# Kernel optimization log

Hardware: AMD Instinct MI355X
Metric: run time of the kernel (lower is better)

## Reference

```python
import jax, jax.numpy as jnp
import numpy as np

N = 8192          # total nodes (bipartite: first half left, second half right)
E = 65536         # raw edges
D = 256           # emb_dim
H = 8             # heads
HD = D // H       # head_dim = 32
EAD = 2           # edge_attr_dim


def _init(k, shape, fan_in):
    return (jax.random.normal(k, shape, jnp.float32) / np.sqrt(fan_in)).astype(jnp.float32)


def setup_inputs() -> dict:
    key = jax.random.key(0)
    ks = jax.random.split(key, 16)
    x = jax.random.normal(ks[0], (N, D), jnp.float32)
    src = jax.random.randint(ks[1], (E,), 0, N // 2, jnp.int32)
    dst = jax.random.randint(ks[2], (E,), N // 2, N, jnp.int32)
    edge_index = jnp.stack([src, dst])                       # [2, E]
    edge_attr = jax.random.uniform(ks[3], (E, EAD), jnp.float32)
    query_mask = jax.random.randint(ks[4], (E,), 0, 2, jnp.int32).astype(bool)
    return {
        "x": x,
        "edge_index": edge_index,
        "edge_attr": edge_attr,
        "query_mask": query_mask,
        "start_right": N // 2,
        "W_kqv": _init(ks[5], (D, 3 * D), D), "b_kqv": jnp.zeros((3 * D,), jnp.float32),
        "W_edge": _init(ks[6], (EAD, D), EAD), "b_edge": jnp.zeros((D,), jnp.float32),
        "W_att1": _init(ks[7], (3 * HD, HD), 3 * HD), "b_att1": jnp.zeros((HD,), jnp.float32),
        "W_att2": _init(ks[8], (HD, 1), HD), "b_att2": jnp.zeros((1,), jnp.float32),
        "W_out": _init(ks[9], (D, D), D), "b_out": jnp.zeros((D,), jnp.float32),
        "bn_gamma": jnp.ones((D,), jnp.float32), "bn_beta": jnp.zeros((D,), jnp.float32),
    }


def _build_graph(edge_index, query_mask, n):
    """Replicates MetaGNN.forward edge preprocessing (static, int-only)."""
    ei = np.asarray(edge_index)
    qm = np.asarray(query_mask).astype(bool)
    sup = np.where(~qm)[0]                                   # support edges
    # cat([edge_index[:, support], edge_index.flip(0)], dim=1)
    src = np.concatenate([ei[0, sup], ei[1]])
    dst = np.concatenate([ei[1, sup], ei[0]])
    attr_idx = np.concatenate([sup, np.arange(ei.shape[1])])
    # remove_self_loops
    keep = src != dst
    src, dst, attr_idx = src[keep], dst[keep], attr_idx[keep]
    # add_self_loops with fill_value [0, 0]
    loops = np.arange(n)
    src = np.concatenate([src, loops])
    dst = np.concatenate([dst, loops])
    return jnp.asarray(src), jnp.asarray(dst), jnp.asarray(attr_idx)


def _layer(x, src, dst, ea, W_kqv, b_kqv, W_edge, b_edge, W_att1, b_att1,
           W_att2, b_att2, W_out, b_out, bn_gamma, bn_beta):
    n = x.shape[0]
    kqv = x @ W_kqv + b_kqv                                  # [N, 3D]
    q = kqv[dst, :D].reshape(-1, H, HD)                      # x_i (target)
    k = kqv[src, D:2 * D].reshape(-1, H, HD) / np.sqrt(HD)   # x_j (source)
    v = kqv[src, 2 * D:].reshape(-1, H, HD)
    ef = jax.nn.relu((ea @ W_edge + b_edge).reshape(-1, H, HD))
    feat = jnp.concatenate([k, q, ef], axis=-1)              # [E, H, 3*HD]
    hdn = jax.nn.relu(jnp.einsum('ehf,fd->ehd', feat, W_att1) + b_att1)
    logits = (jnp.einsum('ehd,do->eho', hdn, W_att2) + b_att2)[..., 0]  # [E, H]
    # scatter-softmax over destination node segments
    m = jax.ops.segment_max(logits, dst, num_segments=n)
    a = jnp.exp(logits - m[dst])
    s = jax.ops.segment_sum(a, dst, num_segments=n)
    alpha = a / (s[dst] + 1e-16)                             # [E, H]
    msg = (alpha[..., None] * v).reshape(-1, D) @ W_out + b_out
    out = jax.ops.segment_sum(msg, dst, num_segments=n) + x  # aggr='add' + residual
    # BatchNorm1d (training-mode batch statistics, eps=1e-5)
    mu = out.mean(axis=0)
    var = out.var(axis=0)
    return (out - mu) / jnp.sqrt(var + 1e-5) * bn_gamma + bn_beta


def reference(x, edge_index, edge_attr, query_mask, start_right,
              W_kqv, b_kqv, W_edge, b_edge, W_att1, b_att1, W_att2, b_att2,
              W_out, b_out, bn_gamma, bn_beta):
    n = x.shape[0]
    src, dst, attr_idx = _build_graph(edge_index, query_mask, n)
    ea = jnp.concatenate(
        [edge_attr[attr_idx], jnp.zeros((n, edge_attr.shape[1]), edge_attr.dtype)], axis=0)
    return _layer(x, src, dst, ea, W_kqv, b_kqv, W_edge, b_edge,
                  W_att1, b_att1, W_att2, b_att2, W_out, b_out, bn_gamma, bn_beta)
```

## Files before the change

### kernel.cpp

```cpp
#include <hip/hip_runtime.h>

#define N_NODES 8192
#define E_RAW   65536
#define NSLOT   (2*E_RAW + N_NODES)
#define DEGCAP  48
#define L_ITER  4
#define MAIN_BLKS (E_RAW / (16 * L_ITER))
#define TAIL_BLKS (N_NODES / (16 * L_ITER))

typedef __attribute__((ext_vector_type(8)))  short bf16x8;
typedef __attribute__((ext_vector_type(4)))  short bf16x4;
typedef __attribute__((ext_vector_type(4)))  float f32x4;
typedef __attribute__((ext_vector_type(16))) float f32x16;
typedef unsigned short u16;

__device__ __forceinline__ u16 f2b(float f) {
  unsigned u = __float_as_uint(f);
  u = (u + 0x7FFFu + ((u >> 16) & 1u)) >> 16;
  return (u16)u;
}
__device__ __forceinline__ float b2f(u16 b) {
  return __uint_as_float(((unsigned)b) << 16);
}

__device__ __forceinline__ bf16x4 kq_rd(const char* wbase, int p, int h, int off) {
  int byte = (p*512 + h*64 + off*2) ^ ((p & 7) << 4);
  return *(const bf16x4*)(wbase + byte);
}

__global__ __launch_bounds__(256) void setup_k(
    const float* __restrict__ x, u16* __restrict__ xb,
    const float* __restrict__ W_kqv, const float* __restrict__ b_kqv,
    const float* __restrict__ W_att1, const float* __restrict__ b_att1,
    const float* __restrict__ W_edge, const float* __restrict__ b_edge,
    const float* __restrict__ W_out,
    u16* __restrict__ BcatT, float* __restrict__ biascat,
    u16* __restrict__ wa1t, u16* __restrict__ WoutT, float* __restrict__ beW,
    int4* __restrict__ zbase)
{
  __shared__ float tile[64][65];
  const float inv_sqrt_hd = 0.17677669529663687f;
  int bx = blockIdx.x, t = threadIdx.x;

  if (bx < 2048) {
    int i = bx * 256 + t;
    float4 v = ((const float4*)x)[i];
    ushort4 o;
    o.x = f2b(v.x); o.y = f2b(v.y); o.z = f2b(v.z); o.w = f2b(v.w);
    ((ushort4*)xb)[i] = o;
    return;
  }
  if (bx < 2836) {
    int c = bx - 2048;
    int i = t;
    if (c < 768) {
      float v;
      if (c < 256) {
        int h = c >> 5, d2 = c & 31;
        float s = 0.f;
        #pragma unroll
        for (int j = 0; j < 32; ++j)
          s += W_kqv[i*768 + 256 + h*32 + j] * W_att1[j*32 + d2];
        v = s * inv_sqrt_hd;
      } else if (c < 512) {
        int c2 = c - 256; int h = c2 >> 5, d2 = c2 & 31;
        float s = 0.f;
        #pragma unroll
        for (int j = 0; j < 32; ++j)
          s += W_kqv[i*768 + h*32 + j] * W_att1[(32+j)*32 + d2];
        v = s;
      } else {
        v = W_kqv[i*768 + c];
      }
      BcatT[(size_t)c * 256 + i] = f2b(v);
      if (i == 0) {
        float bv;
        if (c < 256) {
          int h = c >> 5, d2 = c & 31;
          float s = 0.f;
          for (int j = 0; j < 32; ++j)
            s += b_kqv[256 + h*32 + j] * W_att1[j*32 + d2];
          bv = s * inv_sqrt_hd;
        } else if (c < 512) {
          int c2 = c - 256; int h = c2 >> 5, d2 = c2 & 31;
          float s = 0.f;
          for (int j = 0; j < 32; ++j)
            s += b_kqv[h*32 + j] * W_att1[(32+j)*32 + d2];
          bv = s + b_att1[c2 & 31];
        } else {
          bv = b_kqv[c];
        }
        biascat[c] = bv;
      }
    } else if (c < 772) {
      int idx = (c - 768) * 256 + i;
      int d2 = idx >> 5, j = idx & 31;
      wa1t[idx] = f2b(W_att1[(64 + j) * 32 + d2]);
    } else {
      int b = c - 772;
      int r0 = (b >> 2) * 64, c0 = (b & 3) * 64;
      for (int idx = i; idx < 4096; idx += 256) {
        int r = idx >> 6, cc = idx & 63;
        tile[r][cc] = W_out[(size_t)(r0 + r) * 256 + c0 + cc];
      }
      __syncthreads();
      for (int idx = i; idx < 4096; idx += 256) {
        int cc = idx >> 6, r = idx & 63;
        WoutT[(size_t)(c0 + cc) * 256 + r0 + r] = f2b(tile[r][cc]);
      }
    }
    return;
  }
  if (bx == 2836) {
    int h = t >> 5, d2 = t & 31;
    float s = 0.f;
    #pragma unroll
    for (int f = 0; f < 32; ++f)
      s += fmaxf(b_edge[h*32 + f], 0.f) * W_att1[(64 + f)*32 + d2];
    beW[h*32 + d2] = s;
    return;
  }
  int i = (bx - 2837) * 256 + t;
  if (i < 2176) zbase[i] = make_int4(0, 0, 0, 0);
}

__global__ __launch_bounds__(256) void gemm_scatter_k(
    const u16* __restrict__ xb, const u16* __restrict__ BcatT,
    const float* __restrict__ biascat, u16* __restrict__ nodeF,
    const int* __restrict__ ei, const int* __restrict__ qm,
    int* __restrict__ cnt, int* __restrict__ csr)
{
  int bx = blockIdx.x, t = threadIdx.x;
  if (bx < 768) {
    int lane = t & 63, wid = t >> 6;
    int cb = bx % 12, rb = bx / 12;
    int r0 = rb * 128 + wid * 32;
    int c0 = cb * 64;
    int lr = lane & 15, lk = (lane >> 4) * 8;
    f32x4 acc0[4] = {}, acc1[4] = {};
    for (int k0 = 0; k0 < 256; k0 += 32) {
      bf16x8 a0 = *(const bf16x8*)&xb[(size_t)(r0 + lr) * 256 + k0 + lk];
      bf16x8 a1 = *(const bf16x8*)&xb[(size_t)(r0 + 16 + lr) * 256 + k0 + lk];
      bf16x8 b0 = *(const bf16x8*)&BcatT[(size_t)(c0 + lr) * 256 + k0 + lk];
      bf16x8 b1 = *(const bf16x8*)&BcatT[(size_t)(c0 + 16 + lr) * 256 + k0 + lk];
      bf16x8 b2 = *(const bf16x8*)&BcatT[(size_t)(c0 + 32 + lr) * 256 + k0 + lk];
      bf16x8 b3 = *(const bf16x8*)&BcatT[(size_t)(c0 + 48 + lr) * 256 + k0 + lk];
      acc0[0] = __builtin_amdgcn_mfma_f32_16x16x32_bf16(a0, b0, acc0[0], 0, 0, 0);
      acc0[1] = __builtin_amdgcn_mfma_f32_16x16x32_bf16(a0, b1, acc0[1], 0, 0, 0);
      acc0[2] = __builtin_amdgcn_mfma_f32_16x16x32_bf16(a0, b2, acc0[2], 0, 0, 0);
      acc0[3] = __builtin_amdgcn_mfma_f32_16x16x32_bf16(a0, b3, acc0[3], 0, 0, 0);
      acc1[0] = __builtin_amdgcn_mfma_f32_16x16x32_bf16(a1, b0, acc1[0], 0, 0, 0);
      acc1[1] = __builtin_amdgcn_mfma_f32_16x16x32_bf16(a1, b1, acc1[1], 0, 0, 0);
      acc1[2] = __builtin_amdgcn_mfma_f32_16x16x32_bf16(a1, b2, acc1[2], 0, 0, 0);
      acc1[3] = __builtin_amdgcn_mfma_f32_16x16x32_bf16(a1, b3, acc1[3], 0, 0, 0);
    }
    int rbase = r0 + (lane >> 4) * 4;
    #pragma unroll
    for (int cc = 0; cc < 4; ++cc) {
      float bias = biascat[c0 + cc*16 + lr];
      #pragma unroll
      for (int r = 0; r < 4; ++r) {
        nodeF[(size_t)(rbase + r) * 768 + c0 + cc*16 + lr]      = f2b(acc0[cc][r] + bias);
        nodeF[(size_t)(rbase + 16 + r) * 768 + c0 + cc*16 + lr] = f2b(acc1[cc][r] + bias);
      }
    }
    return;
  }
  int slot = (bx - 768) * 256 + t;
  if (slot >= NSLOT) return;
  int src, dst;
  if (slot < E_RAW) {
    if (qm[slot] != 0) return;
    src = ei[slot]; dst = ei[E_RAW + slot];
  } else if (slot < 2*E_RAW) {
    int e = slot - E_RAW;
    src = ei[E_RAW + e]; dst = ei[e];
  } else {
    int n = slot - 2*E_RAW;
    src = n; dst = n;
  }
  int pos = atomicAdd(&cnt[dst], 1);
  if (pos < DEGCAP) csr[dst*DEGCAP + pos] = (slot << 13) | src;
}

__global__ __launch_bounds__(256) void logits_k(
    const int* __restrict__ ei, const int* __restrict__ qm,
    const float* __restrict__ eattr, const u16* __restrict__ nf,
    const u16* __restrict__ wa1t,
    const float* __restrict__ W_edge, const float* __restrict__ b_edge,
    const float* __restrict__ W_att2, const float* __restrict__ beW,
    float* __restrict__ lgd)
{
  __shared__ __align__(16) char kq_raw[4][16*512];

  int bx = blockIdx.x, t = threadIdx.x, lane = t & 63, wid = t >> 6;
  int col = lane & 31;
  int e = col >> 3, h = col & 7, hi = lane >> 5;
  char* wbase = kq_raw[wid];

  float w2r[16];
  #pragma unroll
  for (int r = 0; r < 16; ++r)
    w2r[r] = W_att2[(r & 3) + 8*(r >> 2) + 4*hi];

  if (bx < MAIN_BLKS) {
    float ce0[16], ce1[16], cbe[16];
    #pragma unroll
    for (int i = 0; i < 8; ++i) {
      int fA = hi*8 + i, fB = 16 + hi*8 + i;
      ce0[i]   = W_edge[h*32 + fA];       ce0[8+i] = W_edge[h*32 + fB];
      ce1[i]   = W_edge[256 + h*32 + fA]; ce1[8+i] = W_edge[256 + h*32 + fB];
      cbe[i]   = b_edge[h*32 + fA];       cbe[8+i] = b_edge[h*32 + fB];
    }
    bf16x8 af0 = *(const bf16x8*)&wa1t[(lane & 31)*32 + hi*8];
    bf16x8 af1 = *(const bf16x8*)&wa1t[(lane & 31)*32 + 16 + hi*8];

    int eqm_r[L_ITER]; float2 ea_r[L_ITER];
    #pragma unroll
    for (int it = 0; it < L_ITER; ++it) {
      int er = ((bx * L_ITER + it) * 4 + wid) * 4 + e;
      eqm_r[it] = qm[er];
      ea_r[it] = *(const float2*)&eattr[2*er];
    }

    #pragma unroll
    for (int it = 0; it < L_ITER; ++it) {
      asm volatile("s_waitcnt lgkmcnt(0)" ::: "memory");
      __builtin_amdgcn_sched_barrier(0);
      #pragma unroll
      for (int m = 0; m < 8; ++m) {
        int erow = ((bx * L_ITER + it) * 4 + wid) * 4 + (m & 3);
        int node = (m >> 2) ? ei[E_RAW + erow] : ei[erow];
        int lo = ((m >> 2) << 2) + (m & 3);
        int p = 2*lo + hi;
        unsigned goff = (unsigned)((lane & 31) * 16) ^ (unsigned)((p & 7) << 4);
        const char* src = (const char*)nf + (size_t)node*1536 + (size_t)hi*512 + goff;
        __builtin_amdgcn_global_load_lds(
            (const __attribute__((address_space(1))) void*)src,
            (__attribute__((address_space(3))) void*)(wbase + lo*1024), 16, 0, 0);
      }

      float2 ea = ea_r[it];
      bf16x8 bf0, bf1;
      #pragma unroll
      for (int i = 0; i < 8; ++i) {
        float v0 = fmaf(ea.x, ce0[i],   fmaf(ea.y, ce1[i],   cbe[i]));
        float v1 = fmaf(ea.x, ce0[8+i], fmaf(ea.y, ce1[8+i], cbe[8+i]));
        bf0[i] = (short)f2b(fmaxf(v0, 0.f));
        bf1[i] = (short)f2b(fmaxf(v1, 0.f));
      }
      f32x16 acc = {};
      acc = __builtin_amdgcn_mfma_f32_32x32x16_bf16(af0, bf0, acc, 0, 0, 0);
      acc = __builtin_amdgcn_mfma_f32_32x32x16_bf16(af1, bf1, acc, 0, 0, 0);

      asm volatile("s_waitcnt vmcnt(0)" ::: "memory");
      __builtin_amdgcn_sched_barrier(0);
      __builtin_amdgcn_wave_barrier();

      float lg0 = 0.f, lg1 = 0.f;
      #pragma unroll
      for (int q = 0; q < 4; ++q) {
        int off = q*8 + 4*hi;
        bf16x4 k0 = kq_rd(wbase, 2*e,     h, off);
        bf16x4 q0 = kq_rd(wbase, 2*e + 9, h, off);
        bf16x4 k1 = kq_rd(wbase, 2*e + 8, h, off);
        bf16x4 q1 = kq_rd(wbase, 2*e + 1, h, off);
        #pragma unroll
        for (int j = 0; j < 4; ++j) {
          int r = q*4 + j;
          float efw = acc[r];
          float p0 = efw + b2f((u16)k0[j]) + b2f((u16)q0[j]);
          float p1 = efw + b2f((u16)k1[j]) + b2f((u16)q1[j]);
          lg0 = fmaf(fmaxf(p0, 0.f), w2r[r], lg0);
          lg1 = fmaf(fmaxf(p1, 0.f), w2r[r], lg1);
        }
      }
      lg0 += __shfl_xor(lg0, 32);
      lg1 += __shfl_xor(lg1, 32);
      int er = ((bx * L_ITER + it) * 4 + wid) * 4 + e;
      if (hi == 0) {
        if (eqm_r[it] == 0) lgd[(size_t)er*8 + h] = lg0;
      } else {
        lgd[(size_t)(E_RAW + er)*8 + h] = lg1;
      }
      __builtin_amdgcn_wave_barrier();
    }
  } else {
    float bew[16];
    #pragma unroll
    for (int r = 0; r < 16; ++r)
      bew[r] = beW[h*32 + (r & 3) + 8*(r >> 2) + 4*hi];

    for (int it = 0; it < L_ITER; ++it) {
      int n0 = (((bx - MAIN_BLKS) * L_ITER + it) * 4 + wid) * 4;
      int nn = n0 + e;
      asm volatile("s_waitcnt lgkmcnt(0)" ::: "memory");
      __builtin_amdgcn_sched_barrier(0);
      #pragma unroll
      for (int m = 0; m < 4; ++m) {
        int node = n0 + m;
        int p = 2*m + hi;
        unsigned goff = (unsigned)((lane & 31) * 16) ^ (unsigned)((p & 7) << 4);
        const char* src = (const char*)nf + (size_t)node*1536 + (size_t)hi*512 + goff;
        __builtin_amdgcn_global_load_lds(
            (const __attribute__((address_space(1))) void*)src,
            (__attribute__((address_space(3))) void*)(wbase + m*1024), 16, 0, 0);
      }
      asm volatile("s_waitcnt vmcnt(0)" ::: "memory");
      __builtin_amdgcn_sched_barrier(0);
      __builtin_amdgcn_wave_barrier();
      float lg0 = 0.f;
      #pragma unroll
      for (int q = 0; q < 4; ++q) {
        int off = q*8 + 4*hi;
        bf16x4 k0 = kq_rd(wbase, 2*e,     h, off);
        bf16x4 q0 = kq_rd(wbase, 2*e + 1, h, off);
        #pragma unroll
        for (int j = 0; j < 4; ++j) {
          int r = q*4 + j;
          float p = bew[r] + b2f((u16)k0[j]) + b2f((u16)q0[j]);
          lg0 = fmaf(fmaxf(p, 0.f), w2r[r], lg0);
        }
      }
      lg0 += __shfl_xor(lg0, 32);
      if (hi == 0) lgd[(size_t)(2*E_RAW + nn)*8 + h] = lg0;
      __builtin_amdgcn_wave_barrier();
    }
  }
}

__global__ __launch_bounds__(256) void aggr_k(const int* __restrict__ cnt,
                                              const int* __restrict__ csr,
                                              const float* __restrict__ lgd,
                                              const u16* __restrict__ nf,
                                              u16* __restrict__ aggb) {
  int t = threadIdx.x, lane = t & 63, wid = t >> 6;
  int n = blockIdx.x * 4 + wid;
  int deg = cnt[n]; if (deg > DEGCAP) deg = DEGCAP;
  int head = lane >> 3;

  int pk = (lane < deg) ? csr[n*DEGCAP + lane] : 0;

  const u16* vb = nf + 512 + lane * 4;
  int pk0 = __shfl(pk, 0);
  float lg_pf = lgd[(size_t)((unsigned)pk0 >> 13)*8 + head];
  bf16x4 v_pf = *(const bf16x4*)&vb[(size_t)(pk0 & 8191) * 768];

  float m = -3.4e38f, s = 0.f;
  float ac0 = 0.f, ac1 = 0.f, ac2 = 0.f, ac3 = 0.f;
  for (int i = 0; i < deg; ++i) {
    float lgv = lg_pf;
    bf16x4 v = v_pf;
    if (i + 1 < deg) {
      int pkn = __shfl(pk, i + 1);
      lg_pf = lgd[(size_t)((unsigned)pkn >> 13)*8 + head];
      v_pf = *(const bf16x4*)&vb[(size_t)(pkn & 8191) * 768];
    }
    float mn = fmaxf(m, lgv);
    float r = __expf(m - mn);
    float a = __expf(lgv - mn);
    s  = fmaf(s, r, a);
    ac0 = fmaf(ac0, r, a * b2f((u16)v[0]));
    ac1 = fmaf(ac1, r, a * b2f((u16)v[1]));
    ac2 = fmaf(ac2, r, a * b2f((u16)v[2]));
    ac3 = fmaf(ac3, r, a * b2f((u16)v[3]));
    m = mn;
  }
  float sinv = 1.f / (s + 1e-16f);
  ushort4 o;
  o.x = f2b(ac0 * sinv); o.y = f2b(ac1 * sinv);
  o.z = f2b(ac2 * sinv); o.w = f2b(ac3 * sinv);
  *(ushort4*)&aggb[(size_t)n * 256 + lane * 4] = o;
}

__global__ __launch_bounds__(256) void gemmout_k(const u16* __restrict__ aggb,
                                                 const u16* __restrict__ WoutT,
                                                 const float* __restrict__ x,
                                                 const int* __restrict__ cnt,
                                                 const float* __restrict__ b_out,
                                                 float* __restrict__ out,
                                                 float* __restrict__ bnsum,
                                                 float* __restrict__ bnsq) {
  int t = threadIdx.x, lane = t & 63, wid = t >> 6;
  int bx = blockIdx.x;
  int cb = bx & 3, rb = bx >> 2;
  int r0 = rb * 128 + wid * 32;
  int c0 = cb * 64;
  int lr = lane & 15, lk = (lane >> 4) * 8;
  f32x4 acc0[4] = {}, acc1[4] = {};
  for (int k0 = 0; k0 < 256; k0 += 32) {
    bf16x8 a0 = *(const bf16x8*)&aggb[(size_t)(r0 + lr) * 256 + k0 + lk];
    bf16x8 a1 = *(const bf16x8*)&aggb[(size_t)(r0 + 16 + lr) * 256 + k0 + lk];
    bf16x8 b0 = *(const bf16x8*)&WoutT[(size_t)(c0 + lr) * 256 + k0 + lk];
    bf16x8 b1 = *(const bf16x8*)&WoutT[(size_t)(c0 + 16 + lr) * 256 + k0 + lk];
    bf16x8 b2 = *(const bf16x8*)&WoutT[(size_t)(c0 + 32 + lr) * 256 + k0 + lk];
    bf16x8 b3 = *(const bf16x8*)&WoutT[(size_t)(c0 + 48 + lr) * 256 + k0 + lk];
    acc0[0] = __builtin_amdgcn_mfma_f32_16x16x32_bf16(a0, b0, acc0[0], 0, 0, 0);
    acc0[1] = __builtin_amdgcn_mfma_f32_16x16x32_bf16(a0, b1, acc0[1], 0, 0, 0);
    acc0[2] = __builtin_amdgcn_mfma_f32_16x16x32_bf16(a0, b2, acc0[2], 0, 0, 0);
    acc0[3] = __builtin_amdgcn_mfma_f32_16x16x32_bf16(a0, b3, acc0[3], 0, 0, 0);
    acc1[0] = __builtin_amdgcn_mfma_f32_16x16x32_bf16(a1, b0, acc1[0], 0, 0, 0);
    acc1[1] = __builtin_amdgcn_mfma_f32_16x16x32_bf16(a1, b1, acc1[1], 0, 0, 0);
    acc1[2] = __builtin_amdgcn_mfma_f32_16x16x32_bf16(a1, b2, acc1[2], 0, 0, 0);
    acc1[3] = __builtin_amdgcn_mfma_f32_16x16x32_bf16(a1, b3, acc1[3], 0, 0, 0);
  }
  int rbase = r0 + (lane >> 4) * 4;
  float degA[4], degB[4];
  #pragma unroll
  for (int r = 0; r < 4; ++r) {
    degA[r] = (float)cnt[rbase + r];
    degB[r] = (float)cnt[rbase + 16 + r];
  }
  #pragma unroll
  for (int cc = 0; cc < 4; ++cc) {
    int colC = c0 + cc*16 + lr;
    float bC = b_out[colC];
    float sC = 0.f, qC = 0.f;
    #pragma unroll
    for (int r = 0; r < 4; ++r) {
      int rowA = rbase + r, rowB = rbase + 16 + r;
      float v0 = acc0[cc][r] + x[(size_t)rowA * 256 + colC] + degA[r] * bC;
      float v1 = acc1[cc][r] + x[(size_t)rowB * 256 + colC] + degB[r] * bC;
      out[(size_t)rowA * 256 + colC] = v0;
      out[(size_t)rowB * 256 + colC] = v1;
      sC += v0 + v1; qC += v0*v0 + v1*v1;
    }
    #pragma unroll
    for (int msk = 16; msk <= 32; msk <<= 1) {
      sC += __shfl_xor(sC, msk); qC += __shfl_xor(qC, msk);
    }
    if (lane < 16) {
      atomicAdd(&bnsum[colC], sC); atomicAdd(&bnsq[colC], qC);
    }
  }
}

__global__ __launch_bounds__(256) void bnapply_k(float* __restrict__ out,
                                                 const float* __restrict__ bnsum,
                                                 const float* __restrict__ bnsq,
                                                 const float* __restrict__ gamma,
                                                 const float* __restrict__ beta) {
  int t = threadIdx.x;
  int c4 = t & 63;
  int r = blockIdx.x * 4 + (t >> 6);
  float4 s4 = ((const float4*)bnsum)[c4];
  float4 q4 = ((const float4*)bnsq)[c4];
  float4 g4 = ((const float4*)gamma)[c4];
  float4 b4 = ((const float4*)beta)[c4];
  float4 v = ((const float4*)out)[(size_t)r * 64 + c4];
  #pragma unroll
  for (int j = 0; j < 4; ++j) {
    float mu = (&s4.x)[j] * (1.f / 8192.f);
    float var = (&q4.x)[j] * (1.f / 8192.f) - mu*mu;
    float inv = rsqrtf(var + 1e-5f);
    (&v.x)[j] = ((&v.x)[j] - mu) * inv * (&g4.x)[j] + (&b4.x)[j];
  }
  ((float4*)out)[(size_t)r * 64 + c4] = v;
}

extern "C" void kernel_launch(void* const* d_in, const int* in_sizes, int n_in,
                              void* d_out, int out_size, void* d_ws, size_t ws_size,
                              hipStream_t stream) {
  (void)in_sizes; (void)n_in; (void)out_size; (void)ws_size;
  const float* x      = (const float*)d_in[0];
  const int*   ei     = (const int*)d_in[1];
  const float* eattr  = (const float*)d_in[2];
  const int*   qm     = (const int*)d_in[3];
  const float* W_kqv  = (const float*)d_in[5];
  const float* b_kqv  = (const float*)d_in[6];
  const float* W_edge = (const float*)d_in[7];
  const float* b_edge = (const float*)d_in[8];
  const float* W_att1 = (const float*)d_in[9];
  const float* b_att1 = (const float*)d_in[10];
  const float* W_att2 = (const float*)d_in[11];
  const float* W_out  = (const float*)d_in[13];
  const float* b_out  = (const float*)d_in[14];
  const float* gamma  = (const float*)d_in[15];
  const float* beta   = (const float*)d_in[16];
  float* out = (float*)d_out;

  char* w = (char*)d_ws;
  u16*    xb      = (u16*)w;     w += (size_t)N_NODES*256*2;
  u16*    BcatT   = (u16*)w;     w += (size_t)768*256*2;
  u16*    wa1t    = (u16*)w;     w += 1024*2;
  u16*    WoutT   = (u16*)w;     w += (size_t)256*256*2;
  u16*    nodeFb  = (u16*)w;     w += (size_t)N_NODES*768*2;
  float*  biascat = (float*)w;   w += 768*4;
  float*  beW     = (float*)w;   w += 256*4;
  u16*    aggb    = (u16*)w;     w += (size_t)N_NODES*256*2;
  int*    cnt     = (int*)w;     w += N_NODES*4;
  float*  bnsum   = (float*)w;   w += 256*4;
  float*  bnsq    = (float*)w;   w += 256*4;
  int*    csr     = (int*)w;     w += (size_t)N_NODES*DEGCAP*4;
  float*  lgd     = (float*)w;   w += (size_t)NSLOT*8*4;

  setup_k<<<2846, 256, 0, stream>>>(
      x, xb, W_kqv, b_kqv, W_att1, b_att1, W_edge, b_edge, W_out,
      BcatT, biascat, wa1t, WoutT, beW, (int4*)cnt);

  gemm_scatter_k<<<768 + (NSLOT + 255)/256, 256, 0, stream>>>(
      xb, BcatT, biascat, nodeFb, ei, qm, cnt, csr);

  logits_k<<<MAIN_BLKS + TAIL_BLKS, 256, 0, stream>>>(
      ei, qm, eattr, nodeFb, wa1t, W_edge, b_edge, W_att2, beW, lgd);

  aggr_k<<<N_NODES/4, 256, 0, stream>>>(cnt, csr, lgd, nodeFb, aggb);

  gemmout_k<<<256, 256, 0, stream>>>(
      aggb, WoutT, x, cnt, b_out, out, bnsum, bnsq);

  bnapply_k<<<N_NODES/4, 256, 0, stream>>>(out, bnsum, bnsq, gamma, beta);
}
```

Before: 96.32 us.

## Double-buffer node-feature LDS loads in logits kernel with 2-wave blocks

Rewrites the logits kernel's main loop so the gathered key/query rows for the next iteration are fetched into a second LDS buffer while the current one is computed, using partial vmcnt waits. Edge indices are read up front as int4 vectors, and blocks shrink from 4 to 2 waves, doubling the grid. The query-mask check is dropped, so logits for query edges are now written unconditionally; those slots are presumably never read through the CSR. This trades more LDS per wave and more register pressure for hiding gather latency.

Result: no change. 94.94 us, median of 2 (-1.4%).

```diff
diff --git a/kernel.cpp b/kernel.cpp
--- a/kernel.cpp
+++ b/kernel.cpp
@@ -5,8 +5,8 @@
 #define NSLOT   (2*E_RAW + N_NODES)
 #define DEGCAP  48
 #define L_ITER  4
-#define MAIN_BLKS (E_RAW / (16 * L_ITER))
-#define TAIL_BLKS (N_NODES / (16 * L_ITER))
+#define MAIN_BLKS (E_RAW / (8 * L_ITER))
+#define TAIL_BLKS (N_NODES / (8 * L_ITER))
 
 typedef __attribute__((ext_vector_type(8)))  short bf16x8;
 typedef __attribute__((ext_vector_type(4)))  short bf16x4;
@@ -183,20 +183,19 @@
   if (pos < DEGCAP) csr[dst*DEGCAP + pos] = (slot << 13) | src;
 }
 
-__global__ __launch_bounds__(256) void logits_k(
-    const int* __restrict__ ei, const int* __restrict__ qm,
+__global__ __launch_bounds__(128) void logits_k(
+    const int* __restrict__ ei,
     const float* __restrict__ eattr, const u16* __restrict__ nf,
     const u16* __restrict__ wa1t,
     const float* __restrict__ W_edge, const float* __restrict__ b_edge,
     const float* __restrict__ W_att2, const float* __restrict__ beW,
     float* __restrict__ lgd)
 {
-  __shared__ __align__(16) char kq_raw[4][16*512];
+  __shared__ __align__(16) char kq_raw[2][2][8192];
 
   int bx = blockIdx.x, t = threadIdx.x, lane = t & 63, wid = t >> 6;
   int col = lane & 31;
   int e = col >> 3, h = col & 7, hi = lane >> 5;
-  char* wbase = kq_raw[wid];
 
   float w2r[16];
   #pragma unroll
@@ -215,30 +214,49 @@
     bf16x8 af0 = *(const bf16x8*)&wa1t[(lane & 31)*32 + hi*8];
     bf16x8 af1 = *(const bf16x8*)&wa1t[(lane & 31)*32 + 16 + hi*8];
 
-    int eqm_r[L_ITER]; float2 ea_r[L_ITER];
+    float2 ea_r[L_ITER];
+    int4 nsv[L_ITER], ndv[L_ITER];
     #pragma unroll
     for (int it = 0; it < L_ITER; ++it) {
-      int er = ((bx * L_ITER + it) * 4 + wid) * 4 + e;
-      eqm_r[it] = qm[er];
-      ea_r[it] = *(const float2*)&eattr[2*er];
-    }
-
-    #pragma unroll
-    for (int it = 0; it < L_ITER; ++it) {
-      asm volatile("s_waitcnt lgkmcnt(0)" ::: "memory");
-      __builtin_amdgcn_sched_barrier(0);
+      int er0 = ((bx * L_ITER + it) * 2 + wid) * 4;
+      ea_r[it] = *(const float2*)&eattr[2*(er0 + e)];
+      nsv[it] = *(const int4*)&ei[er0];
+      ndv[it] = *(const int4*)&ei[E_RAW + er0];
+    }
+
+    unsigned lbase = (unsigned)((lane & 31) * 16);
+    __builtin_amdgcn_sched_barrier(0);
+    {
+      char* base = kq_raw[wid][0];
       #pragma unroll
       for (int m = 0; m < 8; ++m) {
-        int erow = ((bx * L_ITER + it) * 4 + wid) * 4 + (m & 3);
-        int node = (m >> 2) ? ei[E_RAW + erow] : ei[erow];
-        int lo = ((m >> 2) << 2) + (m & 3);
-        int p = 2*lo + hi;
-        unsigned goff = (unsigned)((lane & 31) * 16) ^ (unsigned)((p & 7) << 4);
+        int node = (m >> 2) ? ((&ndv[0].x)[m & 3]) : ((&nsv[0].x)[m & 3]);
+        int p = 2*m + hi;
+        unsigned goff = lbase ^ (unsigned)((p & 7) << 4);
         const char* src = (const char*)nf + (size_t)node*1536 + (size_t)hi*512 + goff;
         __builtin_amdgcn_global_load_lds(
             (const __attribute__((address_space(1))) void*)src,
-            (__attribute__((address_space(3))) void*)(wbase + lo*1024), 16, 0, 0);
-      }
+            (__attribute__((address_space(3))) void*)(base + m*1024), 16, 0, 0);
+      }
+    }
+    __builtin_amdgcn_sched_barrier(0);
+
+    #pragma unroll
+    for (int it = 0; it < L_ITER; ++it) {
+      if (it + 1 < L_ITER) {
+        char* base = kq_raw[wid][(it + 1) & 1];
+        #pragma unroll
+        for (int m = 0; m < 8; ++m) {
+          int node = (m >> 2) ? ((&ndv[it+1].x)[m & 3]) : ((&nsv[it+1].x)[m & 3]);
+          int p = 2*m + hi;
+          unsigned goff = lbase ^ (unsigned)((p & 7) << 4);
+          const char* src = (const char*)nf + (size_t)node*1536 + (size_t)hi*512 + goff;
+          __builtin_amdgcn_global_load_lds(
+              (const __attribute__((address_space(1))) void*)src,
+              (__attribute__((address_space(3))) void*)(base + m*1024), 16, 0, 0);
+        }
+      }
+      __builtin_amdgcn_sched_barrier(0);
 
       float2 ea = ea_r[it];
       bf16x8 bf0, bf1;
@@ -253,10 +271,12 @@
       acc = __builtin_amdgcn_mfma_f32_32x32x16_bf16(af0, bf0, acc, 0, 0, 0);
       acc = __builtin_amdgcn_mfma_f32_32x32x16_bf16(af1, bf1, acc, 0, 0, 0);
 
-      asm volatile("s_waitcnt vmcnt(0)" ::: "memory");
       __builtin_amdgcn_sched_barrier(0);
-      __builtin_amdgcn_wave_barrier();
-
+      if (it + 1 < L_ITER) asm volatile("s_waitcnt vmcnt(8)" ::: "memory");
+      else                 asm volatile("s_waitcnt vmcnt(1)" ::: "memory");
+      __builtin_amdgcn_sched_barrier(0);
+
+      const char* wbase = kq_raw[wid][it & 1];
       float lg0 = 0.f, lg1 = 0.f;
       #pragma unroll
       for (int q = 0; q < 4; ++q) {
@@ -277,13 +297,10 @@
       }
       lg0 += __shfl_xor(lg0, 32);
       lg1 += __shfl_xor(lg1, 32);
-      int er = ((bx * L_ITER + it) * 4 + wid) * 4 + e;
-      if (hi == 0) {
-        if (eqm_r[it] == 0) lgd[(size_t)er*8 + h] = lg0;
-      } else {
-        lgd[(size_t)(E_RAW + er)*8 + h] = lg1;
-      }
-      __builtin_amdgcn_wave_barrier();
+      int er = ((bx * L_ITER + it) * 2 + wid) * 4 + e;
+      size_t soff = hi ? ((size_t)(E_RAW + er)*8 + h) : ((size_t)er*8 + h);
+      lgd[soff] = hi ? lg1 : lg0;
+      __builtin_amdgcn_sched_barrier(0);
     }
   } else {
     float bew[16];
@@ -291,30 +308,28 @@
     for (int r = 0; r < 16; ++r)
       bew[r] = beW[h*32 + (r & 3) + 8*(r >> 2) + 4*hi];
 
+    unsigned lbase = (unsigned)((lane & 31) * 16);
+    char* base = kq_raw[wid][0];
     for (int it = 0; it < L_ITER; ++it) {
-      int n0 = (((bx - MAIN_BLKS) * L_ITER + it) * 4 + wid) * 4;
+      int n0 = (((bx - MAIN_BLKS) * L_ITER + it) * 2 + wid) * 4;
       int nn = n0 + e;
-      asm volatile("s_waitcnt lgkmcnt(0)" ::: "memory");
-      __builtin_amdgcn_sched_barrier(0);
       #pragma unroll
       for (int m = 0; m < 4; ++m) {
-        int node = n0 + m;
         int p = 2*m + hi;
-        unsigned goff = (unsigned)((lane & 31) * 16) ^ (unsigned)((p & 7) << 4);
-        const char* src = (const char*)nf + (size_t)node*1536 + (size_t)hi*512 + goff;
+        unsigned goff = lbase ^ (unsigned)((p & 7) << 4);
+        const char* src = (const char*)nf + (size_t)(n0 + m)*1536 + (size_t)hi*512 + goff;
         __builtin_amdgcn_global_load_lds(
             (const __attribute__((address_space(1))) void*)src,
-            (__attribute__((address_space(3))) void*)(wbase + m*1024), 16, 0, 0);
+            (__attribute__((address_space(3))) void*)(base + m*1024), 16, 0, 0);
       }
       asm volatile("s_waitcnt vmcnt(0)" ::: "memory");
       __builtin_amdgcn_sched_barrier(0);
-      __builtin_amdgcn_wave_barrier();
       float lg0 = 0.f;
       #pragma unroll
       for (int q = 0; q < 4; ++q) {
         int off = q*8 + 4*hi;
-        bf16x4 k0 = kq_rd(wbase, 2*e,     h, off);
-        bf16x4 q0 = kq_rd(wbase, 2*e + 1, h, off);
+        bf16x4 k0 = kq_rd(base, 2*e,     h, off);
+        bf16x4 q0 = kq_rd(base, 2*e + 1, h, off);
         #pragma unroll
         for (int j = 0; j < 4; ++j) {
           int r = q*4 + j;
@@ -324,7 +339,7 @@
       }
       lg0 += __shfl_xor(lg0, 32);
       if (hi == 0) lgd[(size_t)(2*E_RAW + nn)*8 + h] = lg0;
-      __builtin_amdgcn_wave_barrier();
+      __builtin_amdgcn_sched_barrier(0);
     }
   }
 }
@@ -501,8 +516,8 @@
   gemm_scatter_k<<<768 + (NSLOT + 255)/256, 256, 0, stream>>>(
       xb, BcatT, biascat, nodeFb, ei, qm, cnt, csr);
 
-  logits_k<<<MAIN_BLKS + TAIL_BLKS, 256, 0, stream>>>(
-      ei, qm, eattr, nodeFb, wa1t, W_edge, b_edge, W_att2, beW, lgd);
+  logits_k<<<MAIN_BLKS + TAIL_BLKS, 128, 0, stream>>>(
+      ei, eattr, nodeFb, wa1t, W_edge, b_edge, W_att2, beW, lgd);
 
   aggr_k<<<N_NODES/4, 256, 0, stream>>>(cnt, csr, lgd, nodeFb, aggb);
 
```
